# Optimization experiments

Measured on AMD Instinct MI355X. Metric: run time of the kernel, lower is better.

## Reference

```python
import jax, jax.numpy as jnp
import numpy as np

N = 8192          # number of prototypes
D = 128           # proto_dim == hidden_dim (residual requires equality)
H = 2             # GAT heads
K = 3             # k_neighbors + 1 (k_neighbors=2 hard-coded in forward)
NEG_SLOPE = 0.2   # PyG GATConv default leaky relu slope
LN_EPS = 1e-5


def setup_inputs() -> dict:
    key = jax.random.key(0)
    ks = jax.random.split(key, 6)
    prototypes = jax.random.normal(ks[0], (N, D), dtype=jnp.float32)
    labels = jax.random.randint(ks[1], (N,), 0, 1024, dtype=jnp.int64)
    # GATConv params: lin maps D -> H*D (concat=False => per-head dim = hidden_dim)
    W = jax.random.normal(ks[2], (D, H * D), dtype=jnp.float32) / np.sqrt(D)
    att_src = jax.random.normal(ks[3], (H, D), dtype=jnp.float32) / np.sqrt(D)
    att_dst = jax.random.normal(ks[4], (H, D), dtype=jnp.float32) / np.sqrt(D)
    bias = jnp.zeros((D,), dtype=jnp.float32)
    gamma = jnp.ones((D,), dtype=jnp.float32)   # LayerNorm weight
    beta = jnp.zeros((D,), dtype=jnp.float32)   # LayerNorm bias
    return {"prototypes": prototypes, "labels": labels, "W": W,
            "att_src": att_src, "att_dst": att_dst, "bias": bias,
            "gamma": gamma, "beta": beta}


def _knn_edges(x):
    # Squared euclidean distances (same ordering as torch.cdist -> same topk indices).
    sq = jnp.sum(x * x, axis=-1)
    d2 = sq[:, None] + sq[None, :] - 2.0 * (x @ x.T)          # [N, N]
    _, idx = jax.lax.top_k(-d2, K)                            # [N, K] smallest dists
    # topk includes self (dist 0); module masks self-edges then GATConv re-adds
    # self loops, so the effective edge set is exactly the topk set -> static E=N*K.
    src = jnp.repeat(jnp.arange(x.shape[0]), K)               # edge source j
    dst = idx.reshape(-1)                                     # edge target i
    return src, dst


def _gat(x, src, dst, W, att_src, att_dst, bias):
    n = x.shape[0]
    xp = (x @ W).reshape(n, H, D)                             # [N, H, C]
    a_s = jnp.sum(xp * att_src[None], axis=-1)                # [N, H]
    a_d = jnp.sum(xp * att_dst[None], axis=-1)                # [N, H]
    e = a_s[src] + a_d[dst]                                   # [E, H]
    e = jax.nn.leaky_relu(e, NEG_SLOPE)
    # segment softmax over incoming edges of each destination node
    m = jax.ops.segment_max(e, dst, num_segments=n)           # [N, H]
    w = jnp.exp(e - m[dst])
    denom = jax.ops.segment_sum(w, dst, num_segments=n)       # [N, H]
    alpha = w / denom[dst]                                    # [E, H]
    msg = alpha[:, :, None] * xp[src]                         # [E, H, C]
    out = jax.ops.segment_sum(msg, dst, num_segments=n)       # [N, H, C]
    return out.mean(axis=1) + bias                            # concat=False -> head mean


def reference(prototypes, labels, W, att_src, att_dst, bias, gamma, beta):
    x = prototypes
    src, dst = _knn_edges(x)
    x_new = _gat(x, src, dst, W, att_src, att_dst, bias)
    mu = jnp.mean(x_new, axis=-1, keepdims=True)
    var = jnp.var(x_new, axis=-1, keepdims=True)
    x_new = (x_new - mu) * jax.lax.rsqrt(var + LN_EPS) * gamma + beta
    x_new = jax.nn.relu(x_new)
    # dropout layers are identity in eval mode
    return x + x_new
```

## Files before the change

kernel.cpp:

```cpp
#include <hip/hip_runtime.h>
#include <hip/hip_bf16.h>
#include <math.h>

#define GN 8192
#define GD 128
#define GH 2
#define GK 3
#define NEG_SLOPE 0.2f
#define LN_EPS 1e-5f

using short8  = __attribute__((ext_vector_type(8)))  short;
using float16 = __attribute__((ext_vector_type(16))) float;
using f32x4   = __attribute__((ext_vector_type(4)))  float;

__device__ __forceinline__ float wred(float v) {
    #pragma unroll
    for (int o = 32; o > 0; o >>= 1) v += __shfl_xor(v, o, 64);
    return v;
}

__device__ __forceinline__ unsigned fenc(float f) {
    unsigned b = __float_as_uint(f);
    return (b & 0x80000000u) ? ~b : (b | 0x80000000u);
}

__device__ __forceinline__ float rawbf2f(unsigned short s) {
    return __uint_as_float(((unsigned)s) << 16);
}
__device__ __forceinline__ unsigned short f2rawbf(float f) {
    __hip_bfloat16 b = __float2bfloat16(f);
    unsigned short r; __builtin_memcpy(&r, &b, 2);
    return r;
}
__device__ __forceinline__ unsigned umin2(unsigned a, unsigned b) { return a < b ? a : b; }
__device__ __forceinline__ unsigned umax2(unsigned a, unsigned b) { return a > b ? a : b; }

__global__ void k_pre(const float* __restrict__ W, const float* __restrict__ att_src,
                      const float* __restrict__ att_dst,
                      unsigned short* __restrict__ Wth, unsigned short* __restrict__ Wtl,
                      float* __restrict__ uvec) {
    __shared__ float vs[128];
    int b = blockIdx.x, t = threadIdx.x;
    if (b < 128) {
        int e = b * 256 + t;
        int d = e >> 8, j = e & 255;
        int h = j >> 7, c = j & 127;
        int k = h * 128 + d;
        float w = W[e];
        unsigned short hi = f2rawbf(w);
        Wth[c * 256 + k] = hi;
        Wtl[c * 256 + k] = f2rawbf(w - rawbf2f(hi));
    } else {
        int bb = b - 128;
        int h = bb & 1;
        const float* v = (bb < 2 ? att_src : att_dst) + h * 128;
        if (t < 128) vs[t] = v[t];
        __syncthreads();
        int d = t >> 1, half = t & 1;
        const float* wr = W + (size_t)d * 256 + h * 128 + half * 64;
        float s = 0.f;
        for (int c = 0; c < 64; c++) s += wr[c] * vs[half * 64 + c];
        s += __shfl_xor(s, 1, 64);
        if (half == 0) uvec[bb * 128 + d] = s;
    }
}

__global__ void k_conv(const float* __restrict__ x, const float* __restrict__ uvec,
                       float* __restrict__ sq,
                       unsigned short* __restrict__ xa, unsigned short* __restrict__ xb,
                       float* __restrict__ a_s, float* __restrict__ a_d,
                       int* __restrict__ cnt, int* __restrict__ curs) {
    int row = blockIdx.x * 4 + (threadIdx.x >> 6);
    int lane = threadIdx.x & 63;
    const float* xr = x + (size_t)row * GD;
    float a0 = xr[lane], a1 = xr[lane + 64];
    float s = wred(a0 * a0 + a1 * a1);
    unsigned short* ar = xa + (size_t)row * 144;
    unsigned short* br = xb + (size_t)row * 144;
    ar[lane] = f2rawbf(-2.f * a0); ar[lane + 64] = f2rawbf(-2.f * a1);
    br[lane] = f2rawbf(a0);        br[lane + 64] = f2rawbf(a1);
    float s0 = wred(a0 * uvec[lane]       + a1 * uvec[64 + lane]);
    float s1 = wred(a0 * uvec[128 + lane] + a1 * uvec[192 + lane]);
    float d0 = wred(a0 * uvec[256 + lane] + a1 * uvec[320 + lane]);
    float d1 = wred(a0 * uvec[384 + lane] + a1 * uvec[448 + lane]);
    if (lane < 16) {
        unsigned short av = 0, bv = 0;
        if (lane == 0)      { av = f2rawbf(s + 512.f); bv = 0x3F80; }
        else if (lane == 1) { float hi = rawbf2f(f2rawbf(s + 512.f));
                              av = f2rawbf(s + 512.f - hi); bv = 0x3F80; }
        ar[128 + lane] = av; br[128 + lane] = bv;
        if (lane == 0) {
            sq[row] = s;
            a_s[row * 2] = s0; a_s[row * 2 + 1] = s1;
            a_d[row * 2] = d0; a_d[row * 2 + 1] = d1;
            cnt[row] = 0; curs[row] = 0;
        }
    }
}

#define INS(U0,U1,U2,U3,kk) do {                                   \
    unsigned m0_ = umax2(U0,(kk)); U0 = umin2(U0,(kk));            \
    unsigned m1_ = umax2(U1,m0_);  U1 = umin2(U1,m0_);             \
    unsigned m2_ = umax2(U2,m1_);  U2 = umin2(U2,m1_);             \
    U3 = umin2(U3,m2_); } while(0)

#define TOPK16(A, U0,U1,U2,U3, rbase) do {                                        \
    _Pragma("unroll")                                                             \
    for (int q4_ = 0; q4_ < 4; q4_++) {                                           \
        unsigned c0_ = __float_as_uint((A)[q4_ * 4 + 0]);                         \
        unsigned c1_ = __float_as_uint((A)[q4_ * 4 + 1]);                         \
        unsigned c2_ = __float_as_uint((A)[q4_ * 4 + 2]);                         \
        unsigned c3_ = __float_as_uint((A)[q4_ * 4 + 3]);                         \
        unsigned qm_ = umin2(umin2(c0_, c1_), umin2(c2_, c3_));                   \
        if ((qm_ & 0xFFFFE000u) <= U3) {                                          \
            INS(U0,U1,U2,U3, (c0_ & 0xFFFFE000u) | (unsigned)((rbase) + 0 + 8 * q4_)); \
            INS(U0,U1,U2,U3, (c1_ & 0xFFFFE000u) | (unsigned)((rbase) + 1 + 8 * q4_)); \
            INS(U0,U1,U2,U3, (c2_ & 0xFFFFE000u) | (unsigned)((rbase) + 2 + 8 * q4_)); \
            INS(U0,U1,U2,U3, (c3_ & 0xFFFFE000u) | (unsigned)((rbase) + 3 + 8 * q4_)); \
        }                                                                         \
    } } while(0)

#define STAGE_HALF(buf, rowbase)                                                  \
    do {                                                                          \
        _Pragma("unroll")                                                         \
        for (int s_ = 0; s_ < 5; s_++) {                                          \
            if (s_ < 4 || t < 128) {                                              \
                int q_ = s_ * 256 + t;           \
                int kb_ = q_ >> 6, r_ = q_ & 63;                                  \
                __builtin_amdgcn_global_load_lds(                                 \
                    (const __attribute__((address_space(1))) unsigned*)           \
                        (xa + (size_t)((rowbase) + r_) * 144 + kb_ * 8),          \
                    (__attribute__((address_space(3))) unsigned*)&At[(buf)][q_ * 8],\
                    16, 0, 0);                                                    \
            }                                                                     \
        }                                                                         \
    } while (0)

__launch_bounds__(256, 4)
__global__ void k_gemm_topk(const unsigned short* __restrict__ xa,
                            const unsigned short* __restrict__ xb,
                            unsigned* __restrict__ cand) {
    __shared__ __align__(16) unsigned short At[2][18 * 64 * 8];
    int t = threadIdx.x;
    int w = t >> 6, lane = t & 63, h = lane >> 5, n = lane & 31;
    int wn = w & 1, wm = w >> 1;
    int colA = blockIdx.x * 128 + wn * 64 + n;
    int colB = colA + 32;
    int sb = blockIdx.y;
    int rb0 = sb * 512;

    short8 bfragA[9], bfragB[9];
    #pragma unroll
    for (int kc = 0; kc < 9; kc++) {
        bfragA[kc] = *(const short8*)(xb + (size_t)colA * 144 + (2 * kc + h) * 8);
        bfragB[kc] = *(const short8*)(xb + (size_t)colB * 144 + (2 * kc + h) * 8);
    }

    STAGE_HALF(0, rb0);
    asm volatile("s_waitcnt vmcnt(0)" ::: "memory");
    __builtin_amdgcn_s_barrier();

    unsigned TA0 = 0xFFFFFFFFu, TA1 = 0xFFFFFFFFu, TA2 = 0xFFFFFFFFu, TA3 = 0xFFFFFFFFu;
    unsigned TB0 = 0xFFFFFFFFu, TB1 = 0xFFFFFFFFu, TB2 = 0xFFFFFFFFu, TB3 = 0xFFFFFFFFu;

    #pragma unroll 1
    for (int ht = 0; ht < 8; ht++) {
        int cur = ht & 1;
        if (ht < 7) STAGE_HALF(cur ^ 1, rb0 + (ht + 1) * 64);

        float16 acc0 = (float16)(0.f), acc1 = (float16)(0.f);

        #pragma unroll
        for (int kc = 0; kc < 9; kc++) {
            short8 a = *(const short8*)&At[cur][(((2 * kc + h) * 64) + wm * 32 + n) * 8];
            acc0 = __builtin_amdgcn_mfma_f32_32x32x16_bf16(a, bfragA[kc], acc0, 0, 0, 0);
            acc1 = __builtin_amdgcn_mfma_f32_32x32x16_bf16(a, bfragB[kc], acc1, 0, 0, 0);
        }

        int rbq = rb0 + ht * 64 + wm * 32 + 4 * h;
        TOPK16(acc0, TA0, TA1, TA2, TA3, rbq);
        TOPK16(acc1, TB0, TB1, TB2, TB3, rbq);

        if (ht < 7) {
            asm volatile("s_waitcnt vmcnt(0)" ::: "memory");
            __builtin_amdgcn_s_barrier();
        }
    }

    uint4* mrg = (uint4*)&At[0][0];
    if (wm == 0) {
        mrg[(wn * 64 + lane) * 2 + 0] = make_uint4(TA0, TA1, TA2, TA3);
        mrg[(wn * 64 + lane) * 2 + 1] = make_uint4(TB0, TB1, TB2, TB3);
    }
    __syncthreads();
    if (wm == 1) {
        uint4 pa = mrg[(wn * 64 + lane) * 2 + 0];
        uint4 pb = mrg[(wn * 64 + lane) * 2 + 1];
        INS(TA0,TA1,TA2,TA3, pa.x); INS(TA0,TA1,TA2,TA3, pa.y);
        INS(TA0,TA1,TA2,TA3, pa.z); INS(TA0,TA1,TA2,TA3, pa.w);
        INS(TB0,TB1,TB2,TB3, pb.x); INS(TB0,TB1,TB2,TB3, pb.y);
        INS(TB0,TB1,TB2,TB3, pb.z); INS(TB0,TB1,TB2,TB3, pb.w);

        unsigned q0 = (unsigned)__shfl_xor((int)TA0, 32), q1 = (unsigned)__shfl_xor((int)TA1, 32),
                 q2 = (unsigned)__shfl_xor((int)TA2, 32), q3 = (unsigned)__shfl_xor((int)TA3, 32);
        INS(TA0,TA1,TA2,TA3, q0); INS(TA0,TA1,TA2,TA3, q1);
        INS(TA0,TA1,TA2,TA3, q2); INS(TA0,TA1,TA2,TA3, q3);
        q0 = (unsigned)__shfl_xor((int)TB0, 32); q1 = (unsigned)__shfl_xor((int)TB1, 32);
        q2 = (unsigned)__shfl_xor((int)TB2, 32); q3 = (unsigned)__shfl_xor((int)TB3, 32);
        INS(TB0,TB1,TB2,TB3, q0); INS(TB0,TB1,TB2,TB3, q1);
        INS(TB0,TB1,TB2,TB3, q2); INS(TB0,TB1,TB2,TB3, q3);

        if (h == 0) {
            *(uint4*)(cand + (size_t)colA * 64 + sb * 4) = make_uint4(TA0, TA1, TA2, TA3);
            *(uint4*)(cand + (size_t)colB * 64 + sb * 4) = make_uint4(TB0, TB1, TB2, TB3);
        }
    }
}

__device__ __forceinline__ int clampN(int v) {
    return v < 0 ? 0 : (v >= GN ? GN - 1 : v);
}

__global__ void k_refine(const unsigned* __restrict__ cand,
                         const float* __restrict__ x, const float* __restrict__ sq,
                         int* __restrict__ fidx, int* __restrict__ cnt) {
    int t = threadIdx.x, wv = t >> 6, lane = t & 63;
    int j = blockIdx.x * 4 + wv;
    int c = lane >> 2, g = lane & 3;

    unsigned key32 = cand[(size_t)j * 64 + lane];
    int myidx = 0;
    #pragma unroll
    for (int r = 0; r < 16; r++) {
        unsigned m = key32;
        #pragma unroll
        for (int o = 32; o > 0; o >>= 1)
            m = umin2(m, (unsigned)__shfl_xor((int)m, o, 64));
        myidx = (c == r) ? (int)(m & 8191u) : myidx;
        key32 = (key32 == m) ? 0xFFFFFFFFu : key32;
    }

    const float* xi = x + (size_t)myidx * GD + g * 32;
    const float* xj = x + (size_t)j * GD + g * 32;
    float p = 0.f;
    #pragma unroll
    for (int d4 = 0; d4 < 8; d4++) {
        float4 a = *(const float4*)(xi + d4 * 4);
        float4 b = *(const float4*)(xj + d4 * 4);
        p += a.x * b.x + a.y * b.y + a.z * b.z + a.w * b.w;
    }
    p += __shfl_xor(p, 1, 64);
    p += __shfl_xor(p, 2, 64);
    float d2 = sq[j] + sq[myidx] - 2.f * p;
    unsigned long long key = ((unsigned long long)fenc(d2) << 32) | (unsigned)myidx;

    int out3[3];
    #pragma unroll
    for (int r = 0; r < 3; r++) {
        unsigned long long k = key;
        #pragma unroll
        for (int o = 4; o <= 32; o <<= 1) {
            unsigned long long other = __shfl_xor(k, o, 64);
            k = k < other ? k : other;
        }
        out3[r] = (int)(unsigned)(k & 8191u);
        key = (key == k) ? ~0ull : key;
    }
    if (lane == 0) {
        int i0 = clampN(out3[0]), i1 = clampN(out3[1]), i2 = clampN(out3[2]);
        fidx[j * 3 + 0] = i0; fidx[j * 3 + 1] = i1; fidx[j * 3 + 2] = i2;
        atomicAdd(&cnt[i0], 1); atomicAdd(&cnt[i1], 1); atomicAdd(&cnt[i2], 1);
    }
}

__global__ void k_scan(const int* __restrict__ cnt, int* __restrict__ offs) {
    __shared__ __align__(16) int buf[8192];
    __shared__ int wtot[4];
    int t = threadIdx.x, wv = t >> 6, lane = t & 63;
    #pragma unroll
    for (int j = 0; j < 8; j++)
        ((int4*)buf)[j * 256 + t] = ((const int4*)cnt)[j * 256 + t];
    __syncthreads();
    int loc[32], s = 0;
    #pragma unroll
    for (int k = 0; k < 32; k++) { loc[k] = s; s += buf[t * 32 + k]; }
    int inc = s;
    #pragma unroll
    for (int d = 1; d < 64; d <<= 1) {
        int nv = __shfl_up(inc, d, 64);
        if (lane >= d) inc += nv;
    }
    if (lane == 63) wtot[wv] = inc;
    __syncthreads();
    int wbase = 0;
    #pragma unroll
    for (int wq = 0; wq < 4; wq++) wbase += (wq < wv) ? wtot[wq] : 0;
    int base = wbase + inc - s;
    #pragma unroll
    for (int k = 0; k < 32; k++) buf[t * 32 + k] = base + loc[k];
    __syncthreads();
    #pragma unroll
    for (int j = 0; j < 8; j++)
        ((int4*)offs)[j * 256 + t] = ((int4*)buf)[j * 256 + t];
    if (t == 255) offs[GN] = wtot[0] + wtot[1] + wtot[2] + wtot[3];
}

__global__ void k_fill(const int* __restrict__ fidx, const int* __restrict__ offs,
                       int* __restrict__ cursor, int* __restrict__ elist,
                       const float* __restrict__ a_s, const float* __restrict__ a_d,
                       float2* __restrict__ ew) {
    int eid = blockIdx.x * 256 + threadIdx.x;
    int i = clampN(fidx[eid]);
    int src = eid / 3;
    float2 as = ((const float2*)a_s)[src];
    float2 ad = ((const float2*)a_d)[i];
    float e0 = as.x + ad.x; e0 = e0 >= 0.f ? e0 : NEG_SLOPE * e0;
    float e1 = as.y + ad.y; e1 = e1 >= 0.f ? e1 : NEG_SLOPE * e1;
    float w0 = expf(e0), w1 = expf(e1);
    int pos = atomicAdd(&cursor[i], 1);
    int slot = offs[i] + pos;
    if (slot < GN * GK) { elist[slot] = src; ew[slot] = make_float2(w0, w1); }
}

__launch_bounds__(512, 4)
__global__ void k_out(const int* __restrict__ offs, const int* __restrict__ elst,
                      const float2* __restrict__ ew,
                      const float* __restrict__ x,
                      const unsigned short* __restrict__ Wth,
                      const unsigned short* __restrict__ Wtl,
                      const float* __restrict__ bias, const float* __restrict__ gamma,
                      const float* __restrict__ beta, float* __restrict__ out) {
    __shared__ unsigned short zh[16][264];
    __shared__ unsigned short zl[16][264];
    __shared__ float os[16][132];
    int t = threadIdx.x, i0 = blockIdx.x * 16;
    int wv = t >> 6, lane = t & 63;
    int eslot = lane >> 3, g = lane & 7;

    #pragma unroll
    for (int pp = 0; pp < 2; pp++) {
        int r = wv * 2 + pp, node = i0 + r;
        int s = offs[node], e = offs[node + 1];
        float acc0[16], acc1[16];
        #pragma unroll
        for (int q = 0; q < 16; q++) { acc0[q] = 0.f; acc1[q] = 0.f; }
        float w0s = 0.f, w1s = 0.f;
        for (int k0 = s; k0 < e; k0 += 8) {
            int k = k0 + eslot;
            bool valid = k < e;
            int j = valid ? elst[k] : 0;
            float2 wv2 = valid ? ew[k] : make_float2(0.f, 0.f);
            const float* xr = x + (size_t)j * GD + g * 16;
            float4 x0 = *(const float4*)(xr);
            float4 x1 = *(const float4*)(xr + 4);
            float4 x2 = *(const float4*)(xr + 8);
            float4 x3 = *(const float4*)(xr + 12);
            float xv[16] = {x0.x, x0.y, x0.z, x0.w, x1.x, x1.y, x1.z, x1.w,
                            x2.x, x2.y, x2.z, x2.w, x3.x, x3.y, x3.z, x3.w};
            #pragma unroll
            for (int q = 0; q < 16; q++) {
                acc0[q] += wv2.x * xv[q];
                acc1[q] += wv2.y * xv[q];
            }
            w0s += wv2.x; w1s += wv2.y;
        }
        #pragma unroll
        for (int m = 8; m <= 32; m <<= 1) {
            #pragma unroll
            for (int q = 0; q < 16; q++) {
                acc0[q] += __shfl_xor(acc0[q], m, 64);
                acc1[q] += __shfl_xor(acc1[q], m, 64);
            }
            w0s += __shfl_xor(w0s, m, 64);
            w1s += __shfl_xor(w1s, m, 64);
        }
        if (lane < 8) {
            float dn0 = 0.5f / w0s, dn1 = 0.5f / w1s;
            #pragma unroll
            for (int q = 0; q < 16; q += 2) {
                float a0 = acc0[q] * dn0, a1 = acc0[q + 1] * dn0;
                unsigned short h0 = f2rawbf(a0), h1 = f2rawbf(a1);
                *(unsigned*)&zh[r][lane * 16 + q] = (unsigned)h0 | ((unsigned)h1 << 16);
                *(unsigned*)&zl[r][lane * 16 + q] =
                    (unsigned)f2rawbf(a0 - rawbf2f(h0)) |
                    ((unsigned)f2rawbf(a1 - rawbf2f(h1)) << 16);
                float b0 = acc1[q] * dn1, b1 = acc1[q + 1] * dn1;
                unsigned short p0 = f2rawbf(b0), p1 = f2rawbf(b1);
                *(unsigned*)&zh[r][128 + lane * 16 + q] = (unsigned)p0 | ((unsigned)p1 << 16);
                *(unsigned*)&zl[r][128 + lane * 16 + q] =
                    (unsigned)f2rawbf(b0 - rawbf2f(p0)) |
                    ((unsigned)f2rawbf(b1 - rawbf2f(p1)) << 16);
            }
        }
    }
    __syncthreads();

    {
        int qd = lane >> 4, an = lane & 15;
        int c = wv * 16 + an;
        f32x4 acc = {0.f, 0.f, 0.f, 0.f};
        #pragma unroll
        for (int s = 0; s < 8; s++) {
            int ko = s * 32 + qd * 8;
            short8 ah = *(const short8*)&zh[an][ko];
            short8 al = *(const short8*)&zl[an][ko];
            short8 bh = *(const short8*)(Wth + (size_t)c * 256 + ko);
            short8 bl = *(const short8*)(Wtl + (size_t)c * 256 + ko);
            acc = __builtin_amdgcn_mfma_f32_16x16x32_bf16(ah, bh, acc, 0, 0, 0);
            acc = __builtin_amdgcn_mfma_f32_16x16x32_bf16(al, bh, acc, 0, 0, 0);
            acc = __builtin_amdgcn_mfma_f32_16x16x32_bf16(ah, bl, acc, 0, 0, 0);
        }
        #pragma unroll
        for (int r = 0; r < 4; r++) os[qd * 4 + r][c] = acc[r];
    }
    __syncthreads();

    #pragma unroll
    for (int pp = 0; pp < 2; pp++) {
        int r = wv * 2 + pp, node = i0 + r;
        float y0 = os[r][lane] + bias[lane];
        float y1 = os[r][lane + 64] + bias[lane + 64];
        float mu = wred(y0 + y1) * (1.f / 128.f);
        float c0 = y0 - mu, c1 = y1 - mu;
        float var = wred(c0 * c0 + c1 * c1) * (1.f / 128.f);
        float rs2 = 1.f / sqrtf(var + LN_EPS);
        float n0 = c0 * rs2 * gamma[lane] + beta[lane];
        float n1 = c1 * rs2 * gamma[lane + 64] + beta[lane + 64];
        n0 = n0 > 0.f ? n0 : 0.f;
        n1 = n1 > 0.f ? n1 : 0.f;
        out[(size_t)node * GD + lane]      = x[(size_t)node * GD + lane] + n0;
        out[(size_t)node * GD + lane + 64] = x[(size_t)node * GD + lane + 64] + n1;
    }
}

extern "C" void kernel_launch(void* const* d_in, const int* in_sizes, int n_in,
                              void* d_out, int out_size, void* d_ws, size_t ws_size,
                              hipStream_t stream) {
    const float* x       = (const float*)d_in[0];
    const float* W       = (const float*)d_in[2];
    const float* att_src = (const float*)d_in[3];
    const float* att_dst = (const float*)d_in[4];
    const float* bias    = (const float*)d_in[5];
    const float* gamma   = (const float*)d_in[6];
    const float* beta    = (const float*)d_in[7];
    float* out = (float*)d_out;

    char* w = (char*)d_ws;
    unsigned short* xa = (unsigned short*)w; w += (size_t)GN * 144 * 2;
    unsigned short* xb = (unsigned short*)w; w += (size_t)GN * 144 * 2;
    unsigned* cand = (unsigned*)w;           w += (size_t)GN * 64 * 4;
    float2* ew  = (float2*)w; w += (size_t)GN * GK * 8;
    unsigned short* Wth = (unsigned short*)w; w += (size_t)256 * 128 * 2;
    unsigned short* Wtl = (unsigned short*)w; w += (size_t)256 * 128 * 2;
    float* uvec = (float*)w; w += (size_t)4 * 128 * 4;
    float* sq   = (float*)w; w += (size_t)GN * 4;
    float* a_s  = (float*)w; w += (size_t)GN * GH * 4;
    float* a_d  = (float*)w; w += (size_t)GN * GH * 4;
    int*   fidx = (int*)w;   w += (size_t)GN * GK * 4;
    int*   cnt  = (int*)w;   w += (size_t)GN * 4;
    int*   curs = (int*)w;   w += (size_t)GN * 4;
    int*   offs = (int*)w;   w += (size_t)(GN + 1) * 4;
    int*   elst = (int*)w;   w += (size_t)GN * GK * 4;
    size_t need = (size_t)((char*)w - (char*)d_ws);
    if (ws_size < need) return;

    k_pre<<<132, 256, 0, stream>>>(W, att_src, att_dst, Wth, Wtl, uvec);
    k_conv<<<GN / 4, 256, 0, stream>>>(x, uvec, sq, xa, xb, a_s, a_d, cnt, curs);
    k_gemm_topk<<<dim3(64, 16), 256, 0, stream>>>(xa, xb, cand);
    k_refine<<<GN / 4, 256, 0, stream>>>(cand, x, sq, fidx, cnt);
    k_scan<<<1, 256, 0, stream>>>(cnt, offs);
    k_fill<<<GN * GK / 256, 256, 0, stream>>>(fidx, offs, curs, elst, a_s, a_d, ew);
    k_out<<<GN / 16, 512, 0, stream>>>(offs, elst, ew, x, Wth, Wtl, bias, gamma, beta, out);
}
```

Baseline: 195.3 us.

## Shrink gemm-topk tiles: one 32-column MFMA per wave, twice as many row splits

The fused distance-GEMM/top-k kernel now gives each wave its own 32 columns and streams 32-row A tiles (256 rows per block) instead of 64-row tiles shared by a 2x2 wave grid. This removes the LDS merge step and the __syncthreads between wave pairs, halves LDS use and register fragments, raises launch bounds to 6 blocks/SM, and doubles the grid's row-split dimension. In exchange each A tile is reused by only one MFMA per wave, and the candidate buffer doubles to 128 entries per column, so the refine kernel must read and reduce twice as many candidates.

```diff
diff --git a/kernel.cpp b/kernel.cpp
--- a/kernel.cpp
+++ b/kernel.cpp
@@ -123,10 +123,10 @@
 #define STAGE_HALF(buf, rowbase)                                                  \
     do {                                                                          \
         _Pragma("unroll")                                                         \
-        for (int s_ = 0; s_ < 5; s_++) {                                          \
-            if (s_ < 4 || t < 128) {                                              \
+        for (int s_ = 0; s_ < 3; s_++) {                                          \
+            if (s_ < 2 || t < 64) {                                               \
                 int q_ = s_ * 256 + t;           \
-                int kb_ = q_ >> 6, r_ = q_ & 63;                                  \
+                int kb_ = q_ >> 5, r_ = q_ & 31;                                  \
                 __builtin_amdgcn_global_load_lds(                                 \
                     (const __attribute__((address_space(1))) unsigned*)           \
                         (xa + (size_t)((rowbase) + r_) * 144 + kb_ * 8),          \
@@ -136,50 +136,43 @@
         }                                                                         \
     } while (0)
 
-__launch_bounds__(256, 4)
+__launch_bounds__(256, 6)
 __global__ void k_gemm_topk(const unsigned short* __restrict__ xa,
                             const unsigned short* __restrict__ xb,
                             unsigned* __restrict__ cand) {
-    __shared__ __align__(16) unsigned short At[2][18 * 64 * 8];
+    __shared__ __align__(16) unsigned short At[2][18 * 32 * 8];
     int t = threadIdx.x;
     int w = t >> 6, lane = t & 63, h = lane >> 5, n = lane & 31;
-    int wn = w & 1, wm = w >> 1;
-    int colA = blockIdx.x * 128 + wn * 64 + n;
-    int colB = colA + 32;
+    int col = blockIdx.x * 128 + w * 32 + n;
     int sb = blockIdx.y;
-    int rb0 = sb * 512;
-
-    short8 bfragA[9], bfragB[9];
-    #pragma unroll
-    for (int kc = 0; kc < 9; kc++) {
-        bfragA[kc] = *(const short8*)(xb + (size_t)colA * 144 + (2 * kc + h) * 8);
-        bfragB[kc] = *(const short8*)(xb + (size_t)colB * 144 + (2 * kc + h) * 8);
-    }
+    int rb0 = sb * 256;
+
+    short8 bfrag[9];
+    #pragma unroll
+    for (int kc = 0; kc < 9; kc++)
+        bfrag[kc] = *(const short8*)(xb + (size_t)col * 144 + (2 * kc + h) * 8);
 
     STAGE_HALF(0, rb0);
     asm volatile("s_waitcnt vmcnt(0)" ::: "memory");
     __builtin_amdgcn_s_barrier();
 
-    unsigned TA0 = 0xFFFFFFFFu, TA1 = 0xFFFFFFFFu, TA2 = 0xFFFFFFFFu, TA3 = 0xFFFFFFFFu;
-    unsigned TB0 = 0xFFFFFFFFu, TB1 = 0xFFFFFFFFu, TB2 = 0xFFFFFFFFu, TB3 = 0xFFFFFFFFu;
+    unsigned T0 = 0xFFFFFFFFu, T1 = 0xFFFFFFFFu, T2 = 0xFFFFFFFFu, T3 = 0xFFFFFFFFu;
 
     #pragma unroll 1
     for (int ht = 0; ht < 8; ht++) {
         int cur = ht & 1;
-        if (ht < 7) STAGE_HALF(cur ^ 1, rb0 + (ht + 1) * 64);
-
-        float16 acc0 = (float16)(0.f), acc1 = (float16)(0.f);
+        if (ht < 7) STAGE_HALF(cur ^ 1, rb0 + (ht + 1) * 32);
+
+        float16 acc = (float16)(0.f);
 
         #pragma unroll
         for (int kc = 0; kc < 9; kc++) {
-            short8 a = *(const short8*)&At[cur][(((2 * kc + h) * 64) + wm * 32 + n) * 8];
-            acc0 = __builtin_amdgcn_mfma_f32_32x32x16_bf16(a, bfragA[kc], acc0, 0, 0, 0);
-            acc1 = __builtin_amdgcn_mfma_f32_32x32x16_bf16(a, bfragB[kc], acc1, 0, 0, 0);
-        }
-
-        int rbq = rb0 + ht * 64 + wm * 32 + 4 * h;
-        TOPK16(acc0, TA0, TA1, TA2, TA3, rbq);
-        TOPK16(acc1, TB0, TB1, TB2, TB3, rbq);
+            short8 a = *(const short8*)&At[cur][(((2 * kc + h) * 32) + n) * 8];
+            acc = __builtin_amdgcn_mfma_f32_32x32x16_bf16(a, bfrag[kc], acc, 0, 0, 0);
+        }
+
+        int rbq = rb0 + ht * 32 + 4 * h;
+        TOPK16(acc, T0, T1, T2, T3, rbq);
 
         if (ht < 7) {
             asm volatile("s_waitcnt vmcnt(0)" ::: "memory");
@@ -187,33 +180,13 @@
         }
     }
 
-    uint4* mrg = (uint4*)&At[0][0];
-    if (wm == 0) {
-        mrg[(wn * 64 + lane) * 2 + 0] = make_uint4(TA0, TA1, TA2, TA3);
-        mrg[(wn * 64 + lane) * 2 + 1] = make_uint4(TB0, TB1, TB2, TB3);
-    }
-    __syncthreads();
-    if (wm == 1) {
-        uint4 pa = mrg[(wn * 64 + lane) * 2 + 0];
-        uint4 pb = mrg[(wn * 64 + lane) * 2 + 1];
-        INS(TA0,TA1,TA2,TA3, pa.x); INS(TA0,TA1,TA2,TA3, pa.y);
-        INS(TA0,TA1,TA2,TA3, pa.z); INS(TA0,TA1,TA2,TA3, pa.w);
-        INS(TB0,TB1,TB2,TB3, pb.x); INS(TB0,TB1,TB2,TB3, pb.y);
-        INS(TB0,TB1,TB2,TB3, pb.z); INS(TB0,TB1,TB2,TB3, pb.w);
-
-        unsigned q0 = (unsigned)__shfl_xor((int)TA0, 32), q1 = (unsigned)__shfl_xor((int)TA1, 32),
-                 q2 = (unsigned)__shfl_xor((int)TA2, 32), q3 = (unsigned)__shfl_xor((int)TA3, 32);
-        INS(TA0,TA1,TA2,TA3, q0); INS(TA0,TA1,TA2,TA3, q1);
-        INS(TA0,TA1,TA2,TA3, q2); INS(TA0,TA1,TA2,TA3, q3);
-        q0 = (unsigned)__shfl_xor((int)TB0, 32); q1 = (unsigned)__shfl_xor((int)TB1, 32);
-        q2 = (unsigned)__shfl_xor((int)TB2, 32); q3 = (unsigned)__shfl_xor((int)TB3, 32);
-        INS(TB0,TB1,TB2,TB3, q0); INS(TB0,TB1,TB2,TB3, q1);
-        INS(TB0,TB1,TB2,TB3, q2); INS(TB0,TB1,TB2,TB3, q3);
-
-        if (h == 0) {
-            *(uint4*)(cand + (size_t)colA * 64 + sb * 4) = make_uint4(TA0, TA1, TA2, TA3);
-            *(uint4*)(cand + (size_t)colB * 64 + sb * 4) = make_uint4(TB0, TB1, TB2, TB3);
-        }
+    unsigned p0 = (unsigned)__shfl_xor((int)T0, 32), p1 = (unsigned)__shfl_xor((int)T1, 32),
+             p2 = (unsigned)__shfl_xor((int)T2, 32), p3 = (unsigned)__shfl_xor((int)T3, 32);
+    INS(T0,T1,T2,T3, p0); INS(T0,T1,T2,T3, p1);
+    INS(T0,T1,T2,T3, p2); INS(T0,T1,T2,T3, p3);
+    if (h == 0) {
+        uint4 o = make_uint4(T0, T1, T2, T3);
+        *(uint4*)(cand + (size_t)col * 128 + sb * 4) = o;
     }
 }
 
@@ -228,16 +201,18 @@
     int j = blockIdx.x * 4 + wv;
     int c = lane >> 2, g = lane & 3;
 
-    unsigned key32 = cand[(size_t)j * 64 + lane];
+    unsigned k0 = cand[(size_t)j * 128 + lane];
+    unsigned k1 = cand[(size_t)j * 128 + 64 + lane];
     int myidx = 0;
     #pragma unroll
     for (int r = 0; r < 16; r++) {
-        unsigned m = key32;
+        unsigned m = umin2(k0, k1);
         #pragma unroll
         for (int o = 32; o > 0; o >>= 1)
             m = umin2(m, (unsigned)__shfl_xor((int)m, o, 64));
         myidx = (c == r) ? (int)(m & 8191u) : myidx;
-        key32 = (key32 == m) ? 0xFFFFFFFFu : key32;
+        k0 = (k0 == m) ? 0xFFFFFFFFu : k0;
+        k1 = (k1 == m) ? 0xFFFFFFFFu : k1;
     }
 
     const float* xi = x + (size_t)myidx * GD + g * 32;
@@ -448,7 +423,7 @@
     char* w = (char*)d_ws;
     unsigned short* xa = (unsigned short*)w; w += (size_t)GN * 144 * 2;
     unsigned short* xb = (unsigned short*)w; w += (size_t)GN * 144 * 2;
-    unsigned* cand = (unsigned*)w;           w += (size_t)GN * 64 * 4;
+    unsigned* cand = (unsigned*)w;           w += (size_t)GN * 128 * 4;
     float2* ew  = (float2*)w; w += (size_t)GN * GK * 8;
     unsigned short* Wth = (unsigned short*)w; w += (size_t)256 * 128 * 2;
     unsigned short* Wtl = (unsigned short*)w; w += (size_t)256 * 128 * 2;
@@ -466,7 +441,7 @@
 
     k_pre<<<132, 256, 0, stream>>>(W, att_src, att_dst, Wth, Wtl, uvec);
     k_conv<<<GN / 4, 256, 0, stream>>>(x, uvec, sq, xa, xb, a_s, a_d, cnt, curs);
-    k_gemm_topk<<<dim3(64, 16), 256, 0, stream>>>(xa, xb, cand);
+    k_gemm_topk<<<dim3(64, 32), 256, 0, stream>>>(xa, xb, cand);
     k_refine<<<GN / 4, 256, 0, stream>>>(cand, x, sq, fidx, cnt);
     k_scan<<<1, 256, 0, stream>>>(cnt, offs);
     k_fill<<<GN * GK / 256, 256, 0, stream>>>(fidx, offs, curs, elst, a_s, a_d, ew);
```

After: 166.7 us. 14.6% less time.
